# Kernel tuning notes

Measured on AMD Instinct MI355X. Metric: run time of the kernel, lower is better.

Reference implementation:

```python
import jax, jax.numpy as jnp
import numpy as np

B, H, W, C = 16, 64, 64, 512
DIM, VDIM = 256, 256

def setup_inputs() -> dict:
    key = jax.random.key(0)
    ks = jax.random.split(key, 5)
    s = 0.02  # small init scale for stable softmax/matmuls
    return {
        "x": jax.random.normal(ks[0], (B, H, W, C), jnp.float32),
        "Wq": jax.random.normal(ks[1], (C, DIM), jnp.float32) * s,
        "bq": jnp.zeros((DIM,), jnp.float32),
        "Wk": jax.random.normal(ks[2], (C, VDIM), jnp.float32) * s,
        "bk": jnp.zeros((VDIM,), jnp.float32),
        "Wv": jax.random.normal(ks[3], (C, VDIM), jnp.float32) * s,
        "bv": jnp.zeros((VDIM,), jnp.float32),
        "Wr": jax.random.normal(ks[4], (DIM, C), jnp.float32) * s,
        "br": jnp.zeros((C,), jnp.float32),
    }

def reference(x, Wq, bq, Wk, bk, Wv, bv, Wr, br):
    b, h, w, c = x.shape
    n = h * w
    # 1x1 convs == per-pixel linear projections
    q = (x @ Wq + bq).reshape(b, n, -1)                      # [b, n, dim]
    k = (x @ Wk + bk).reshape(b, n, -1)                      # [b, n, vdim]
    v = (x @ Wv + bv).reshape(b, n, -1)                      # [b, n, vdim]
    attention_maps = jax.nn.softmax(k, axis=1)               # softmax over positions
    attention_vectors = jax.nn.softmax(v, axis=1)
    # feature gathering: global descriptors [b, vdim, dim]
    global_descriptors = jnp.einsum('bnd,bnv->bvd', q, attention_maps)
    # feature distribution back to positions
    out = jnp.einsum('bvd,bnv->bnd', global_descriptors, attention_vectors)
    out = out.reshape(b, h, w, -1)                           # [b, h, w, dim]
    # reconstruct 1x1 conv dim -> c
    return out @ Wr + br
```

## Files before the change

kernel.cpp:

```cpp
#include <hip/hip_runtime.h>


#define BATCH 16
#define NPOS 4096
#define CDIM 512
#define DDIM 256
#define MTOT (BATCH * NPOS)

typedef unsigned short u16;
typedef __attribute__((ext_vector_type(4))) unsigned short u16x4;
typedef __attribute__((ext_vector_type(8))) unsigned short u16x8;
typedef __attribute__((ext_vector_type(8))) short s16x8;
typedef __attribute__((ext_vector_type(4))) float f32x4;

__device__ __forceinline__ u16 f2bf(float f) {
    union { float f; unsigned u; } v; v.f = f;
    unsigned u = v.u;
    unsigned r = (u + 0x7fffu + ((u >> 16) & 1u)) >> 16;
    return (u16)r;
}
__device__ __forceinline__ float bf2f(u16 h) {
    union { unsigned u; float f; } v; v.u = ((unsigned)h) << 16;
    return v.f;
}

__device__ __forceinline__ void gload_lds16(const u16* g, u16* l) {
    __builtin_amdgcn_global_load_lds(
        (const __attribute__((address_space(1))) void*)g,
        (__attribute__((address_space(3))) void*)l, 16, 0, 0);
}

__device__ __forceinline__ void gemm_core(
    const u16* __restrict__ A, int lda,
    const u16* __restrict__ B, int ldb,
    int m0, int n0, long koff, int ksteps,
    u16* As, u16* Bs, f32x4 (&acc)[4][4])
{
    const int tid  = threadIdx.x;
    const int lane = tid & 63;
    const int wave = tid >> 6;
    const int wm = wave >> 1, wn = wave & 1;
    const int fr = lane & 15;
    const int kq = lane >> 4;

    const int srow = lane >> 2;
    const int skq  = lane & 3;

    const u16* Arow0 = A + (size_t)(m0 + wave * 16 + srow) * lda + koff + skq * 8;
    const u16* Arow1 = A + (size_t)(m0 + 64 + wave * 16 + srow) * lda + koff + skq * 8;
    const u16* Brow0 = B + (size_t)(n0 + wave * 16 + srow) * ldb + koff + skq * 8;
    const u16* Brow1 = B + (size_t)(n0 + 64 + wave * 16 + srow) * ldb + koff + skq * 8;

    u16* AsW0 = As + wave * 512;
    u16* AsW1 = As + 2048 + wave * 512;
    u16* BsW0 = Bs + wave * 512;
    u16* BsW1 = Bs + 2048 + wave * 512;

    for (int ks = 0; ks < ksteps; ++ks) {
        const size_t ko = (size_t)ks * 32;
        __syncthreads();
        gload_lds16(Arow0 + ko, AsW0);
        gload_lds16(Arow1 + ko, AsW1);
        gload_lds16(Brow0 + ko, BsW0);
        gload_lds16(Brow1 + ko, BsW1);
        __syncthreads();

        s16x8 aF[4], bF[4];
#pragma unroll
        for (int i = 0; i < 4; ++i)
            aF[i] = *(const s16x8*)(As + (size_t)(wm * 64 + i * 16 + fr) * 32 + kq * 8);
#pragma unroll
        for (int j = 0; j < 4; ++j)
            bF[j] = *(const s16x8*)(Bs + (size_t)(wn * 64 + j * 16 + fr) * 32 + kq * 8);
#pragma unroll
        for (int i = 0; i < 4; ++i)
#pragma unroll
            for (int j = 0; j < 4; ++j)
                acc[i][j] = __builtin_amdgcn_mfma_f32_16x16x32_bf16(
                    aF[i], bF[j], acc[i][j], 0, 0, 0);
    }
}

__global__ __launch_bounds__(256) void cast_x(const float* __restrict__ x,
                                              u16* __restrict__ xb, int n4)
{
    int i = blockIdx.x * 256 + threadIdx.x;
    const int stride = gridDim.x * 256;
    for (; i < n4; i += stride) {
        float4 f = ((const float4*)x)[i];
        u16x4 o = { f2bf(f.x), f2bf(f.y), f2bf(f.z), f2bf(f.w) };
        ((u16x4*)xb)[i] = o;
    }
}

__global__ __launch_bounds__(256) void cast_w(
    const float* __restrict__ Wq, const float* __restrict__ Wk,
    const float* __restrict__ Wv, const float* __restrict__ bq,
    const float* __restrict__ bk, const float* __restrict__ bv,
    const float* __restrict__ Wr,
    u16* __restrict__ WqkvT, u16* __restrict__ WrT, float* __restrict__ bqkv)
{
    const int i0 = blockIdx.x * 256 + threadIdx.x;
    const int stride = gridDim.x * 256;
    for (int idx = i0; idx < 768 * 512; idx += stride) {
        int nc = idx >> 9, kk = idx & 511;
        const float* W = (nc < 256) ? Wq : (nc < 512) ? Wk : Wv;
        WqkvT[idx] = f2bf(W[(size_t)kk * 256 + (nc & 255)]);
    }
    for (int idx = i0; idx < 512 * 256; idx += stride) {
        int c = idx >> 8, d = idx & 255;
        WrT[idx] = f2bf(Wr[(size_t)d * 512 + c]);
    }
    for (int idx = i0; idx < 768; idx += stride)
        bqkv[idx] = (idx < 256) ? bq[idx] : (idx < 512) ? bk[idx - 256] : bv[idx - 512];
}

__global__ __launch_bounds__(256) void proj_qkv(
    const u16* __restrict__ xb, const u16* __restrict__ WqkvT,
    const float* __restrict__ bqkv,
    u16* __restrict__ qT, u16* __restrict__ kT, u16* __restrict__ vb)
{
    __shared__ u16 smem[18432];
    u16* As = smem;
    u16* Bs = smem + 4096;

    const int bx = blockIdx.x;
    const int n0 = bx * 128;
    const int m0 = blockIdx.y * 128;

    f32x4 acc[4][4];
#pragma unroll
    for (int i = 0; i < 4; ++i)
#pragma unroll
        for (int j = 0; j < 4; ++j) acc[i][j] = (f32x4){0.f, 0.f, 0.f, 0.f};

    gemm_core(xb, 512, WqkvT, 512, m0, n0, 0, 16, As, Bs, acc);

    const int tid = threadIdx.x, lane = tid & 63, wave = tid >> 6;
    const int wm = wave >> 1, wn = wave & 1, fr = lane & 15, kq = lane >> 4;
    const int mode = bx >> 1;
    const int nl0 = (bx & 1) * 128;

    if (mode == 2) {
#pragma unroll
        for (int i = 0; i < 4; ++i)
#pragma unroll
            for (int j = 0; j < 4; ++j) {
                const int col = wn * 64 + j * 16 + fr;
                const float bias = bqkv[n0 + col];
#pragma unroll
                for (int r = 0; r < 4; ++r) {
                    const int row = wm * 64 + i * 16 + kq * 4 + r;
                    vb[(size_t)(m0 + row) * 256 + nl0 + col] = f2bf(acc[i][j][r] + bias);
                }
            }
        return;
    }

    __syncthreads();
    u16* Ts = smem + wave * 4608;
#pragma unroll
    for (int i = 0; i < 4; ++i)
#pragma unroll
        for (int j = 0; j < 4; ++j) {
            const int colw = j * 16 + fr;
            const float bias = bqkv[n0 + wn * 64 + colw];
#pragma unroll
            for (int r = 0; r < 4; ++r) {
                const int roww = i * 16 + kq * 4 + r;
                Ts[roww * 72 + colw] = f2bf(acc[i][j][r] + bias);
            }
        }
    __syncthreads();

    u16* dstT = (mode == 0) ? qT : kT;
    const int b = m0 >> 12;
    const int nbase = (m0 & 4095) + wm * 64;
    const int dch = nl0 + wn * 64 + lane;
    u16* dst = dstT + (size_t)b * (256 * 4096) + (size_t)dch * 4096 + nbase;
#pragma unroll
    for (int g = 0; g < 8; ++g) {
        u16x8 pack;
#pragma unroll
        for (int e = 0; e < 8; ++e)
            pack[e] = Ts[(g * 8 + e) * 72 + lane];
        *(u16x8*)(dst + g * 8) = pack;
    }
}

__global__ __launch_bounds__(256) void ksoftmax(u16* __restrict__ kT)
{
    u16* row = kT + (size_t)blockIdx.x * 4096;
    const int t = threadIdx.x, lane = t & 63, wave = t >> 6;
    __shared__ float red[4];

    float x[16];
    u16x8 u0 = *(const u16x8*)(row + t * 16);
    u16x8 u1 = *(const u16x8*)(row + t * 16 + 8);
#pragma unroll
    for (int e = 0; e < 8; ++e) { x[e] = bf2f(u0[e]); x[8 + e] = bf2f(u1[e]); }

    float m = -3.4e38f;
#pragma unroll
    for (int e = 0; e < 16; ++e) m = fmaxf(m, x[e]);
    for (int off = 32; off; off >>= 1) m = fmaxf(m, __shfl_xor(m, off));
    if (lane == 0) red[wave] = m;
    __syncthreads();
    const float M = fmaxf(fmaxf(red[0], red[1]), fmaxf(red[2], red[3]));
    __syncthreads();

    float s = 0.f;
#pragma unroll
    for (int e = 0; e < 16; ++e) { x[e] = __expf(x[e] - M); s += x[e]; }
    for (int off = 32; off; off >>= 1) s += __shfl_xor(s, off);
    if (lane == 0) red[wave] = s;
    __syncthreads();
    const float inv = 1.f / (red[0] + red[1] + red[2] + red[3]);

    u16x8 o0, o1;
#pragma unroll
    for (int e = 0; e < 8; ++e) { o0[e] = f2bf(x[e] * inv); o1[e] = f2bf(x[8 + e] * inv); }
    *(u16x8*)(row + t * 16) = o0;
    *(u16x8*)(row + t * 16 + 8) = o1;
}

__global__ __launch_bounds__(256) void vsm_partial(
    const u16* __restrict__ vb, float* __restrict__ pmax, float* __restrict__ psum)
{
    const int b = blockIdx.y, chunk = blockIdx.x, ch = threadIdx.x;
    const u16* T = vb + ((size_t)b * 4096 + (size_t)chunk * 128) * 256 + ch;
    float m = -3.4e38f, s = 0.f;
    for (int r = 0; r < 128; ++r) {
        float x = bf2f(T[(size_t)r * 256]);
        float nm = fmaxf(m, x);
        s = s * __expf(m - nm) + __expf(x - nm);
        m = nm;
    }
    const size_t idx = ((size_t)b * 32 + chunk) * 256 + ch;
    pmax[idx] = m; psum[idx] = s;
}

__global__ __launch_bounds__(256) void vsm_combine(
    const float* __restrict__ pmax, const float* __restrict__ psum,
    float* __restrict__ gmax, float* __restrict__ ginv)
{
    const int b = blockIdx.x, ch = threadIdx.x;
    const size_t base = (size_t)b * 32 * 256 + ch;
    float M = -3.4e38f;
    for (int c = 0; c < 32; ++c) M = fmaxf(M, pmax[base + (size_t)c * 256]);
    float s = 0.f;
    for (int c = 0; c < 32; ++c)
        s += psum[base + (size_t)c * 256] * __expf(pmax[base + (size_t)c * 256] - M);
    gmax[(size_t)b * 256 + ch] = M;
    ginv[(size_t)b * 256 + ch] = 1.f / s;
}

__global__ __launch_bounds__(256) void vsm_write(
    u16* __restrict__ vb, const float* __restrict__ gmax, const float* __restrict__ ginv)
{
    const int b = blockIdx.y, chunk = blockIdx.x, ch = threadIdx.x;
    u16* T = vb + ((size_t)b * 4096 + (size_t)chunk * 128) * 256 + ch;
    const float M = gmax[(size_t)b * 256 + ch], R = ginv[(size_t)b * 256 + ch];
    for (int r = 0; r < 128; ++r) {
        float x = bf2f(T[(size_t)r * 256]);
        T[(size_t)r * 256] = f2bf(__expf(x - M) * R);
    }
}

__global__ __launch_bounds__(256) void g_gemm(
    const u16* __restrict__ kT, const u16* __restrict__ qT, float* __restrict__ Gpart)
{
    __shared__ u16 smem[8192];
    const int z = blockIdx.z, b = z >> 3, kc = z & 7;
    const int n0 = blockIdx.x * 128, m0 = blockIdx.y * 128;

    f32x4 acc[4][4];
#pragma unroll
    for (int i = 0; i < 4; ++i)
#pragma unroll
        for (int j = 0; j < 4; ++j) acc[i][j] = (f32x4){0.f, 0.f, 0.f, 0.f};

    gemm_core(kT + (size_t)b * (256 * 4096), 4096,
              qT + (size_t)b * (256 * 4096), 4096,
              m0, n0, (long)kc * 512, 16, smem, smem + 4096, acc);

    float* C = Gpart + (size_t)z * 65536;
    const int lane = threadIdx.x & 63, wave = threadIdx.x >> 6;
    const int wm = wave >> 1, wn = wave & 1, fr = lane & 15, kq = lane >> 4;
#pragma unroll
    for (int i = 0; i < 4; ++i)
#pragma unroll
        for (int j = 0; j < 4; ++j)
#pragma unroll
            for (int r = 0; r < 4; ++r) {
                const int row = wm * 64 + i * 16 + kq * 4 + r;
                const int col = wn * 64 + j * 16 + fr;
                C[(size_t)(m0 + row) * 256 + n0 + col] = acc[i][j][r];
            }
}

__global__ __launch_bounds__(256) void greduce(const float* __restrict__ Gpart,
                                               u16* __restrict__ Gb)
{
    const int i = blockIdx.x * 256 + threadIdx.x;
    const int b = i >> 16, r = i & 65535;
    const float* p = Gpart + (size_t)(b * 8) * 65536 + r;
    float s = 0.f;
#pragma unroll
    for (int kc = 0; kc < 8; ++kc) s += p[(size_t)kc * 65536];
    Gb[i] = f2bf(s);
}

__global__ __launch_bounds__(256) void gwT_gemm(
    const u16* __restrict__ WrT, const u16* __restrict__ Gb, u16* __restrict__ GWT)
{
    __shared__ u16 smem[8192];
    const int b = blockIdx.z;
    const int n0 = blockIdx.x * 128, m0 = blockIdx.y * 128;

    f32x4 acc[4][4];
#pragma unroll
    for (int i = 0; i < 4; ++i)
#pragma unroll
        for (int j = 0; j < 4; ++j) acc[i][j] = (f32x4){0.f, 0.f, 0.f, 0.f};

    gemm_core(WrT, 256, Gb + (size_t)b * 65536, 256, m0, n0, 0, 8,
              smem, smem + 4096, acc);

    u16* C = GWT + (size_t)b * (512 * 256);
    const int lane = threadIdx.x & 63, wave = threadIdx.x >> 6;
    const int wm = wave >> 1, wn = wave & 1, fr = lane & 15, kq = lane >> 4;
#pragma unroll
    for (int i = 0; i < 4; ++i)
#pragma unroll
        for (int j = 0; j < 4; ++j)
#pragma unroll
            for (int r = 0; r < 4; ++r) {
                const int row = wm * 64 + i * 16 + kq * 4 + r;
                const int col = wn * 64 + j * 16 + fr;
                C[(size_t)(m0 + row) * 256 + n0 + col] = f2bf(acc[i][j][r]);
            }
}

__global__ __launch_bounds__(256) void out_gemm(
    const u16* __restrict__ vsm, const u16* __restrict__ GWT,
    const float* __restrict__ br, float* __restrict__ out)
{
    __shared__ u16 smem[8192];
    const int n0 = blockIdx.x * 128, m0 = blockIdx.y * 128;
    const int b = m0 >> 12;

    f32x4 acc[4][4];
#pragma unroll
    for (int i = 0; i < 4; ++i)
#pragma unroll
        for (int j = 0; j < 4; ++j) acc[i][j] = (f32x4){0.f, 0.f, 0.f, 0.f};

    gemm_core(vsm, 256, GWT + (size_t)b * (512 * 256), 256, m0, n0, 0, 8,
              smem, smem + 4096, acc);

    const int lane = threadIdx.x & 63, wave = threadIdx.x >> 6;
    const int wm = wave >> 1, wn = wave & 1, fr = lane & 15, kq = lane >> 4;
#pragma unroll
    for (int i = 0; i < 4; ++i)
#pragma unroll
        for (int j = 0; j < 4; ++j) {
            const int col = wn * 64 + j * 16 + fr;
            const float bias = br[n0 + col];
#pragma unroll
            for (int r = 0; r < 4; ++r) {
                const int row = wm * 64 + i * 16 + kq * 4 + r;
                out[(size_t)(m0 + row) * 512 + n0 + col] = acc[i][j][r] + bias;
            }
        }
}

extern "C" void kernel_launch(void* const* d_in, const int* in_sizes, int n_in,
                              void* d_out, int out_size, void* d_ws, size_t ws_size,
                              hipStream_t stream)
{
    const float* x  = (const float*)d_in[0];
    const float* Wq = (const float*)d_in[1];
    const float* bq = (const float*)d_in[2];
    const float* Wk = (const float*)d_in[3];
    const float* bk = (const float*)d_in[4];
    const float* Wv = (const float*)d_in[5];
    const float* bv = (const float*)d_in[6];
    const float* Wr = (const float*)d_in[7];
    const float* br = (const float*)d_in[8];
    float* out = (float*)d_out;

    char* w = (char*)d_ws;
    u16*   xb    = (u16*)(w);
    u16*   qT    = (u16*)(w + 67108864);
    u16*   kT    = (u16*)(w + 100663296);
    u16*   vb    = (u16*)(w + 134217728);
    float* Gpart = (float*)(w + 167772160);
    u16*   Gb    = (u16*)(w + 201326592);
    u16*   GWT   = (u16*)(w + 203423744);
    u16*   WqkvT = (u16*)(w + 207618048);
    u16*   WrT   = (u16*)(w + 208404480);
    float* bqkv  = (float*)(w + 208666624);
    float* pmax  = (float*)(w + 208669696);
    float* psum  = (float*)(w + 209193984);
    float* gmax  = (float*)(w + 209718272);
    float* ginv  = (float*)(w + 209734656);

    const dim3 blk(256);

    cast_x<<<2048, blk, 0, stream>>>(x, xb, (MTOT * CDIM) / 4);
    cast_w<<<512, blk, 0, stream>>>(Wq, Wk, Wv, bq, bk, bv, Wr, WqkvT, WrT, bqkv);

    proj_qkv<<<dim3(6, 512), blk, 0, stream>>>(xb, WqkvT, bqkv, qT, kT, vb);

    ksoftmax<<<BATCH * 256, blk, 0, stream>>>(kT);
    vsm_partial<<<dim3(32, BATCH), blk, 0, stream>>>(vb, pmax, psum);
    vsm_combine<<<BATCH, blk, 0, stream>>>(pmax, psum, gmax, ginv);
    vsm_write<<<dim3(32, BATCH), blk, 0, stream>>>(vb, gmax, ginv);

    g_gemm<<<dim3(2, 2, BATCH * 8), blk, 0, stream>>>(kT, qT, Gpart);
    greduce<<<4096, blk, 0, stream>>>(Gpart, Gb);

    gwT_gemm<<<dim3(2, 4, BATCH), blk, 0, stream>>>(WrT, Gb, GWT);

    out_gemm<<<dim3(4, 512), blk, 0, stream>>>(vb, GWT, br, out);
}
```

Measured before the change: 464.6 us.

## Double-buffer GEMM LDS tiles, swizzle LDS layout, and remap blocks across XCDs

The shared GEMM core now double-buffers the LDS tiles. It prefetches the k-step two ahead with global_load_lds, using explicit vmcnt waits and raw barriers instead of two full __syncthreads per step. Tile columns are XOR-swizzled to cut LDS bank conflicts on fragment reads, and the proj_qkv transpose staging buffer uses a skewed layout instead of padding. Flat grids for proj_qkv and out_gemm are remapped so consecutive tiles land on the same XCD for L2 reuse. Doubled LDS use per block may lower occupancy.

Result: faster. 426.6 us (-8.2%).

```diff
diff --git a/kernel.cpp b/kernel.cpp
--- a/kernel.cpp
+++ b/kernel.cpp
@@ -30,48 +30,65 @@
         (__attribute__((address_space(3))) void*)l, 16, 0, 0);
 }
 
+__device__ __forceinline__ void stage_tile(
+    const u16* Arow0, const u16* Arow1, const u16* Brow0, const u16* Brow1,
+    u16* As, u16* Bs, int wave, long tko)
+{
+    gload_lds16(Arow0 + tko, As + wave * 512);
+    gload_lds16(Arow1 + tko, As + 2048 + wave * 512);
+    gload_lds16(Brow0 + tko, Bs + wave * 512);
+    gload_lds16(Brow1 + tko, Bs + 2048 + wave * 512);
+}
+
 __device__ __forceinline__ void gemm_core(
     const u16* __restrict__ A, int lda,
     const u16* __restrict__ B, int ldb,
     int m0, int n0, long koff, int ksteps,
-    u16* As, u16* Bs, f32x4 (&acc)[4][4])
-{
-    const int tid  = threadIdx.x;
-    const int lane = tid & 63;
-    const int wave = tid >> 6;
+    u16* smem, f32x4 (&acc)[4][4])
+{
+    const int tid = threadIdx.x, lane = tid & 63, wave = tid >> 6;
     const int wm = wave >> 1, wn = wave & 1;
-    const int fr = lane & 15;
-    const int kq = lane >> 4;
-
-    const int srow = lane >> 2;
-    const int skq  = lane & 3;
-
-    const u16* Arow0 = A + (size_t)(m0 + wave * 16 + srow) * lda + koff + skq * 8;
-    const u16* Arow1 = A + (size_t)(m0 + 64 + wave * 16 + srow) * lda + koff + skq * 8;
-    const u16* Brow0 = B + (size_t)(n0 + wave * 16 + srow) * ldb + koff + skq * 8;
-    const u16* Brow1 = B + (size_t)(n0 + 64 + wave * 16 + srow) * ldb + koff + skq * 8;
-
-    u16* AsW0 = As + wave * 512;
-    u16* AsW1 = As + 2048 + wave * 512;
-    u16* BsW0 = Bs + wave * 512;
-    u16* BsW1 = Bs + 2048 + wave * 512;
-
-    for (int ks = 0; ks < ksteps; ++ks) {
-        const size_t ko = (size_t)ks * 32;
-        __syncthreads();
-        gload_lds16(Arow0 + ko, AsW0);
-        gload_lds16(Arow1 + ko, AsW1);
-        gload_lds16(Brow0 + ko, BsW0);
-        gload_lds16(Brow1 + ko, BsW1);
-        __syncthreads();
+    const int fr = lane & 15, kq = lane >> 4;
+    const int srow = lane >> 2, skq = lane & 3;
+    const int sslot = (skq ^ (srow & 3)) * 8;
+
+    const u16* Arow0 = A + (size_t)(m0 + wave * 16 + srow) * lda + koff + sslot;
+    const u16* Arow1 = A + (size_t)(m0 + 64 + wave * 16 + srow) * lda + koff + sslot;
+    const u16* Brow0 = B + (size_t)(n0 + wave * 16 + srow) * ldb + koff + sslot;
+    const u16* Brow1 = B + (size_t)(n0 + 64 + wave * 16 + srow) * ldb + koff + sslot;
+
+    u16* AsB[2] = { smem,        smem + 8192 };
+    u16* BsB[2] = { smem + 4096, smem + 12288 };
+
+    stage_tile(Arow0, Arow1, Brow0, Brow1, AsB[0], BsB[0], wave, 0);
+    if (ksteps > 1)
+        stage_tile(Arow0, Arow1, Brow0, Brow1, AsB[1], BsB[1], wave, 32);
+
+    const int arow = wm * 64, brow = wn * 64;
+    const int slot = (kq ^ (fr & 3)) * 8;
+
+    for (int t = 0; t < ksteps; ++t) {
+        u16* As = AsB[t & 1];
+        u16* Bs = BsB[t & 1];
+        if (t + 1 < ksteps)
+            asm volatile("s_waitcnt vmcnt(4)" ::: "memory");
+        else
+            asm volatile("s_waitcnt vmcnt(0)" ::: "memory");
+        __builtin_amdgcn_s_barrier();
 
         s16x8 aF[4], bF[4];
 #pragma unroll
         for (int i = 0; i < 4; ++i)
-            aF[i] = *(const s16x8*)(As + (size_t)(wm * 64 + i * 16 + fr) * 32 + kq * 8);
+            aF[i] = *(const s16x8*)(As + (size_t)(arow + i * 16 + fr) * 32 + slot);
 #pragma unroll
         for (int j = 0; j < 4; ++j)
-            bF[j] = *(const s16x8*)(Bs + (size_t)(wn * 64 + j * 16 + fr) * 32 + kq * 8);
+            bF[j] = *(const s16x8*)(Bs + (size_t)(brow + j * 16 + fr) * 32 + slot);
+
+        asm volatile("s_waitcnt lgkmcnt(0)" ::: "memory");
+        __builtin_amdgcn_s_barrier();
+        if (t + 2 < ksteps)
+            stage_tile(Arow0, Arow1, Brow0, Brow1, As, Bs, wave, (long)(t + 2) * 32);
+
 #pragma unroll
         for (int i = 0; i < 4; ++i)
 #pragma unroll
@@ -115,18 +132,23 @@
         bqkv[idx] = (idx < 256) ? bq[idx] : (idx < 512) ? bk[idx - 256] : bv[idx - 512];
 }
 
+__device__ __forceinline__ int tskew(int row, int col) {
+    return row * 64 + (col ^ (((row >> 2) & 3) << 4));
+}
+
 __global__ __launch_bounds__(256) void proj_qkv(
     const u16* __restrict__ xb, const u16* __restrict__ WqkvT,
     const float* __restrict__ bqkv,
     u16* __restrict__ qT, u16* __restrict__ kT, u16* __restrict__ vb)
 {
-    __shared__ u16 smem[18432];
-    u16* As = smem;
-    u16* Bs = smem + 4096;
-
-    const int bx = blockIdx.x;
+    __shared__ u16 smem[16384];
+
+    const int bid = blockIdx.x;
+    const int nid = (bid & 7) * 384 + (bid >> 3);
+    const int bx = nid % 6;
+    const int by = nid / 6;
     const int n0 = bx * 128;
-    const int m0 = blockIdx.y * 128;
+    const int m0 = by * 128;
 
     f32x4 acc[4][4];
 #pragma unroll
@@ -134,7 +156,7 @@
 #pragma unroll
         for (int j = 0; j < 4; ++j) acc[i][j] = (f32x4){0.f, 0.f, 0.f, 0.f};
 
-    gemm_core(xb, 512, WqkvT, 512, m0, n0, 0, 16, As, Bs, acc);
+    gemm_core(xb, 512, WqkvT, 512, m0, n0, 0, 16, smem, acc);
 
     const int tid = threadIdx.x, lane = tid & 63, wave = tid >> 6;
     const int wm = wave >> 1, wn = wave & 1, fr = lane & 15, kq = lane >> 4;
@@ -158,7 +180,7 @@
     }
 
     __syncthreads();
-    u16* Ts = smem + wave * 4608;
+    u16* Ts = smem + wave * 4096;
 #pragma unroll
     for (int i = 0; i < 4; ++i)
 #pragma unroll
@@ -166,10 +188,8 @@
             const int colw = j * 16 + fr;
             const float bias = bqkv[n0 + wn * 64 + colw];
 #pragma unroll
-            for (int r = 0; r < 4; ++r) {
-                const int roww = i * 16 + kq * 4 + r;
-                Ts[roww * 72 + colw] = f2bf(acc[i][j][r] + bias);
-            }
+            for (int r = 0; r < 4; ++r)
+                Ts[tskew(i * 16 + kq * 4 + r, colw)] = f2bf(acc[i][j][r] + bias);
         }
     __syncthreads();
 
@@ -183,7 +203,7 @@
         u16x8 pack;
 #pragma unroll
         for (int e = 0; e < 8; ++e)
-            pack[e] = Ts[(g * 8 + e) * 72 + lane];
+            pack[e] = Ts[tskew(g * 8 + e, lane)];
         *(u16x8*)(dst + g * 8) = pack;
     }
 }
@@ -270,7 +290,7 @@
 __global__ __launch_bounds__(256) void g_gemm(
     const u16* __restrict__ kT, const u16* __restrict__ qT, float* __restrict__ Gpart)
 {
-    __shared__ u16 smem[8192];
+    __shared__ u16 smem[16384];
     const int z = blockIdx.z, b = z >> 3, kc = z & 7;
     const int n0 = blockIdx.x * 128, m0 = blockIdx.y * 128;
 
@@ -282,7 +302,7 @@
 
     gemm_core(kT + (size_t)b * (256 * 4096), 4096,
               qT + (size_t)b * (256 * 4096), 4096,
-              m0, n0, (long)kc * 512, 16, smem, smem + 4096, acc);
+              m0, n0, (long)kc * 512, 16, smem, acc);
 
     float* C = Gpart + (size_t)z * 65536;
     const int lane = threadIdx.x & 63, wave = threadIdx.x >> 6;
@@ -314,7 +334,7 @@
 __global__ __launch_bounds__(256) void gwT_gemm(
     const u16* __restrict__ WrT, const u16* __restrict__ Gb, u16* __restrict__ GWT)
 {
-    __shared__ u16 smem[8192];
+    __shared__ u16 smem[16384];
     const int b = blockIdx.z;
     const int n0 = blockIdx.x * 128, m0 = blockIdx.y * 128;
 
@@ -324,8 +344,7 @@
 #pragma unroll
         for (int j = 0; j < 4; ++j) acc[i][j] = (f32x4){0.f, 0.f, 0.f, 0.f};
 
-    gemm_core(WrT, 256, Gb + (size_t)b * 65536, 256, m0, n0, 0, 8,
-              smem, smem + 4096, acc);
+    gemm_core(WrT, 256, Gb + (size_t)b * 65536, 256, m0, n0, 0, 8, smem, acc);
 
     u16* C = GWT + (size_t)b * (512 * 256);
     const int lane = threadIdx.x & 63, wave = threadIdx.x >> 6;
@@ -346,8 +365,11 @@
     const u16* __restrict__ vsm, const u16* __restrict__ GWT,
     const float* __restrict__ br, float* __restrict__ out)
 {
-    __shared__ u16 smem[8192];
-    const int n0 = blockIdx.x * 128, m0 = blockIdx.y * 128;
+    __shared__ u16 smem[16384];
+    const int bid = blockIdx.x;
+    const int nid = (bid & 7) * 256 + (bid >> 3);
+    const int n0 = (nid & 3) * 128;
+    const int m0 = (nid >> 2) * 128;
     const int b = m0 >> 12;
 
     f32x4 acc[4][4];
@@ -356,8 +378,7 @@
 #pragma unroll
         for (int j = 0; j < 4; ++j) acc[i][j] = (f32x4){0.f, 0.f, 0.f, 0.f};
 
-    gemm_core(vsm, 256, GWT + (size_t)b * (512 * 256), 256, m0, n0, 0, 8,
-              smem, smem + 4096, acc);
+    gemm_core(vsm, 256, GWT + (size_t)b * (512 * 256), 256, m0, n0, 0, 8, smem, acc);
 
     const int lane = threadIdx.x & 63, wave = threadIdx.x >> 6;
     const int wm = wave >> 1, wn = wave & 1, fr = lane & 15, kq = lane >> 4;
@@ -411,7 +432,7 @@
     cast_x<<<2048, blk, 0, stream>>>(x, xb, (MTOT * CDIM) / 4);
     cast_w<<<512, blk, 0, stream>>>(Wq, Wk, Wv, bq, bk, bv, Wr, WqkvT, WrT, bqkv);
 
-    proj_qkv<<<dim3(6, 512), blk, 0, stream>>>(xb, WqkvT, bqkv, qT, kT, vb);
+    proj_qkv<<<3072, blk, 0, stream>>>(xb, WqkvT, bqkv, qT, kT, vb);
 
     ksoftmax<<<BATCH * 256, blk, 0, stream>>>(kT);
     vsm_partial<<<dim3(32, BATCH), blk, 0, stream>>>(vb, pmax, psum);
@@ -423,5 +444,5 @@
 
     gwT_gemm<<<dim3(2, 4, BATCH), blk, 0, stream>>>(WrT, Gb, GWT);
 
-    out_gemm<<<dim3(4, 512), blk, 0, stream>>>(vb, GWT, br, out);
-}
+    out_gemm<<<2048, blk, 0, stream>>>(vb, GWT, br, out);
+}
```
